# Optimization experiments

Hardware: AMD Instinct MI355X
Metric: run time of the kernel (lower is better)

The kernel has to match this reference:

```python
import math
import jax
import jax.numpy as jnp
import numpy as np
from jax import lax

B, L, D = 8, 3072, 512
DM, H, CF = 512, 8, 512
E = DM // H
KSIZE = 25
C_FACTOR = 1


def setup_inputs() -> dict:
    key = jax.random.key(0)
    ks = jax.random.split(key, 16)
    s = lambda fan: 1.0 / np.sqrt(fan)
    inp = {
        "inputs": jax.random.normal(ks[0], (B, L, D), jnp.float32),
        "W_res": jax.random.normal(ks[1], (D, DM), jnp.float32) * s(D),
        "b_res": jnp.zeros((DM,), jnp.float32),
        "W_in": jax.random.normal(ks[2], (DM, DM), jnp.float32) * s(DM),
        "b_in": jnp.zeros((DM,), jnp.float32),
        "Wq": jax.random.normal(ks[3], (DM, DM), jnp.float32) * s(DM),
        "bq": jnp.zeros((DM,), jnp.float32),
        "Wk": jax.random.normal(ks[4], (DM, DM), jnp.float32) * s(DM),
        "bk": jnp.zeros((DM,), jnp.float32),
        "Wv": jax.random.normal(ks[5], (DM, DM), jnp.float32) * s(DM),
        "bv": jnp.zeros((DM,), jnp.float32),
        "Wo": jax.random.normal(ks[6], (DM, DM), jnp.float32) * s(DM),
        "bo": jnp.zeros((DM,), jnp.float32),
        "Wc1": jax.random.normal(ks[7], (DM, CF), jnp.float32) * s(DM),
        "Wc2": jax.random.normal(ks[8], (CF, CF), jnp.float32) * s(CF),
    }
    return inp


def series_decomp(x):
    # moving average with 'same' padding, TF-style (count excludes padding)
    ssum = lax.reduce_window(x, 0.0, lax.add, (1, KSIZE, 1), (1, 1, 1), "SAME")
    cnt = lax.reduce_window(jnp.ones_like(x), 0.0, lax.add, (1, KSIZE, 1), (1, 1, 1), "SAME")
    trend = ssum / cnt
    return x - trend, trend


def auto_correlation(q, k, v):
    # q,k,v: [B, L, H, E]
    qf = jnp.fft.rfft(q, axis=1)
    kf = jnp.fft.rfft(k, axis=1)
    corr = jnp.fft.irfft(qf * jnp.conj(kf), n=L, axis=1)  # [B, L, H, E]
    mean_corr = corr.mean(axis=(2, 3))  # [B, L]
    k_top = int(C_FACTOR * math.log(L))  # = 8
    weights, delays = lax.top_k(mean_corr, k_top)  # [B, k_top]
    w = jax.nn.softmax(weights, axis=-1)  # [B, k_top]
    # gather v rolled by each delay: idx[b,i,l] = (l + delay[b,i]) % L
    idx = (jnp.arange(L)[None, None, :] + delays[:, :, None]) % L  # [B, k_top, L]
    v_rolled = jnp.take_along_axis(v[:, None], idx[:, :, :, None, None], axis=2)  # [B,k,L,H,E]
    return jnp.einsum("bklhe,bk->blhe", v_rolled, w)


def reference(inputs, W_res, b_res, W_in, b_in, Wq, bq, Wk, bk, Wv, bv, Wo, bo, Wc1, Wc2):
    proj = inputs @ W_res + b_res  # [B,L,DM]
    x = proj @ W_in + b_in
    q = (x @ Wq + bq).reshape(B, L, H, E)
    kk = (x @ Wk + bk).reshape(B, L, H, E)
    vv = (x @ Wv + bv).reshape(B, L, H, E)
    attn = auto_correlation(q, kk, vv).reshape(B, L, DM)
    attn = attn @ Wo + bo
    x = attn + proj
    seasonal, _ = series_decomp(x)
    y = jax.nn.relu(seasonal @ Wc1)  # Conv1D kernel_size=1, no bias
    y = y @ Wc2
    out, _ = series_decomp(y)
    return out
```

## Files before the change

### kernel.cpp

```cpp
#include <hip/hip_runtime.h>
#include <hip/hip_bf16.h>


#define LQ 3072
#define DD 512
#define BB 8
#define MTOT (BB * LQ)
#define KTOP 8
#define KSZ 25
#define KHALF 12
#define KK 512
#define KB (KK * 2)

typedef unsigned short ushort_t;
typedef __attribute__((ext_vector_type(4))) float f32x4;
typedef __attribute__((ext_vector_type(8))) short s16x8;
typedef __attribute__((ext_vector_type(4))) short s16x4;

typedef __attribute__((address_space(1))) unsigned int u32_g;
typedef __attribute__((address_space(3))) unsigned int u32_l;

__device__ __forceinline__ ushort_t f2bfbits(float x) {
  __hip_bfloat16 h = __float2bfloat16(x);
  return __builtin_bit_cast(unsigned short, h);
}
__device__ __forceinline__ float bfbits2f(ushort_t s) {
  __hip_bfloat16 h = __builtin_bit_cast(__hip_bfloat16, (unsigned short)s);
  return __bfloat162float(h);
}

__device__ __forceinline__ void gload_lds16(const void* g, void* l) {
  __builtin_amdgcn_global_load_lds((const u32_g*)g, (u32_l*)l, 16, 0, 0);
}

__device__ __forceinline__ void gemm3_core(
    const ushort_t* __restrict__ Ah, const ushort_t* __restrict__ Al,
    const ushort_t* __restrict__ Bh, const ushort_t* __restrict__ Bl,
    int arow0, int brow0, char* lds, f32x4 acc[4][4]) {
  const int tid = threadIdx.x, lane = tid & 63, w = tid >> 6;
  const int wr = w >> 1, wc = w & 1;
  const int c = lane & 15, qd = lane >> 4;

  const ushort_t* ssrc = (w == 0) ? Ah : (w == 1) ? Al : (w == 2) ? Bh : Bl;
  const int srow0 = (w < 2) ? arow0 : brow0;
  const int L0 = lane >> 3, sl = lane & 7;
  const int u = sl ^ L0;
  const char* gbase =
      (const char*)ssrc + (size_t)(srow0 + 2 * L0 + (u >> 2)) * KB + (u & 3) * 16;
  char* ldsT = lds + w * 8192;

  int aoff[4], boff[4];
#pragma unroll
  for (int m = 0; m < 4; m++) {
    int r = wr * 64 + m * 16 + c;
    int L = r >> 1;
    aoff[m] = L * 128 + (((((r & 1) << 2) | qd) ^ (L & 7)) << 4);
    r = wc * 64 + m * 16 + c;
    L = r >> 1;
    boff[m] = 16384 + L * 128 + (((((r & 1) << 2) | qd) ^ (L & 7)) << 4);
  }

#pragma unroll
  for (int m = 0; m < 4; m++)
#pragma unroll
    for (int n = 0; n < 4; n++) acc[m][n] = 0.f;

  for (int k0 = 0; k0 < KK; k0 += 32) {
    __syncthreads();
    const char* g = gbase + k0 * 2;
#pragma unroll
    for (int i = 0; i < 8; i++) gload_lds16(g + (size_t)i * (16 * KB), ldsT + i * 1024);
    __syncthreads();

    s16x8 ah[4], al[4];
#pragma unroll
    for (int m = 0; m < 4; m++) {
      ah[m] = *(const s16x8*)(lds + aoff[m]);
      al[m] = *(const s16x8*)(lds + 8192 + aoff[m]);
    }
#pragma unroll
    for (int n = 0; n < 4; n++) {
      s16x8 bh = *(const s16x8*)(lds + boff[n]);
      s16x8 bl = *(const s16x8*)(lds + 8192 + boff[n]);
#pragma unroll
      for (int m = 0; m < 4; m++) {
        acc[m][n] = __builtin_amdgcn_mfma_f32_16x16x32_bf16(ah[m], bh, acc[m][n], 0, 0, 0);
        acc[m][n] = __builtin_amdgcn_mfma_f32_16x16x32_bf16(ah[m], bl, acc[m][n], 0, 0, 0);
        acc[m][n] = __builtin_amdgcn_mfma_f32_16x16x32_bf16(al[m], bh, acc[m][n], 0, 0, 0);
      }
    }
  }
}

template <int OUTMODE, int RESMODE, int RELU>
__global__ __launch_bounds__(256, 3) void gemm_bf16x3(
    const ushort_t* __restrict__ Ah, const ushort_t* __restrict__ Al,
    const ushort_t* __restrict__ Bh, const ushort_t* __restrict__ Bl,
    const float* __restrict__ bias,
    const ushort_t* __restrict__ resH, const ushort_t* __restrict__ resL,
    float* __restrict__ outF, ushort_t* __restrict__ outH, ushort_t* __restrict__ outL) {
  __shared__ alignas(16) char lds[32768];
  const int m0 = blockIdx.y * 128, n0 = blockIdx.x * 128;
  f32x4 acc[4][4];
  gemm3_core(Ah, Al, Bh, Bl, m0, n0, lds, acc);

  const int tid = threadIdx.x, lane = tid & 63, w = tid >> 6;
  const int wr = w >> 1, wc = w & 1, qd = lane >> 4, c = lane & 15;
#pragma unroll
  for (int m = 0; m < 4; m++)
#pragma unroll
    for (int n = 0; n < 4; n++) {
      int col = n0 + wc * 64 + n * 16 + c;
      float badd = bias ? bias[col] : 0.f;
#pragma unroll
      for (int r = 0; r < 4; r++) {
        int row = m0 + wr * 64 + m * 16 + 4 * qd + r;
        size_t off = (size_t)row * DD + col;
        float val = acc[m][n][r] + badd;
        if (RESMODE == 1) val += bfbits2f(resH[off]) + bfbits2f(resL[off]);
        if (RELU) val = fmaxf(val, 0.f);
        if (OUTMODE == 0) {
          outF[off] = val;
        } else {
          ushort_t h = f2bfbits(val);
          outH[off] = h;
          outL[off] = f2bfbits(val - bfbits2f(h));
        }
      }
    }
}

__global__ __launch_bounds__(256, 3) void corr_gemm(
    const ushort_t* __restrict__ Qh, const ushort_t* __restrict__ Ql,
    const ushort_t* __restrict__ Kh, const ushort_t* __restrict__ Kl,
    float* __restrict__ mc) {
  __shared__ alignas(16) char lds[32768];
  __shared__ float bins[256];
  const int b = blockIdx.z;
  const int m0 = blockIdx.y * 128, n0 = blockIdx.x * 128;
  bins[threadIdx.x] = 0.f;
  f32x4 acc[4][4];
  gemm3_core(Qh, Ql, Kh, Kl, b * LQ + m0, b * LQ + n0, lds, acc);

  const int tid = threadIdx.x, lane = tid & 63, w = tid >> 6;
  const int wr = w >> 1, wc = w & 1, qd = lane >> 4, c = lane & 15;

  float psum[7][4];
#pragma unroll
  for (int d = 0; d < 7; d++)
#pragma unroll
    for (int r = 0; r < 4; r++) psum[d][r] = 0.f;
#pragma unroll
  for (int m = 0; m < 4; m++)
#pragma unroll
    for (int n = 0; n < 4; n++) {
      int d = m - n + 3;
#pragma unroll
      for (int r = 0; r < 4; r++) psum[d][r] += acc[m][n][r];
    }

  __syncthreads();
  const int lanebase = 64 * (wr - wc) + 4 * qd - c + 127;
#pragma unroll
  for (int d = 0; d < 7; d++)
#pragma unroll
    for (int r = 0; r < 4; r++) atomicAdd(&bins[lanebase + 16 * (d - 3) + r], psum[d][r]);
  __syncthreads();

  if (tid < 255) {
    int tau = 128 * ((int)blockIdx.y - (int)blockIdx.x) + tid - 127;
    tau = ((tau % LQ) + LQ) % LQ;
    atomicAdd(&mc[b * LQ + tau], bins[tid]);
  }
}

struct P8 {
  const float* p[8];
};

__global__ void transpose_split(P8 srcs, ushort_t* __restrict__ dH, ushort_t* __restrict__ dL) {
  __shared__ float t[32][33];
  const int i = blockIdx.z;
  const float* src = srcs.p[i];
  const size_t base = (size_t)i * DD * DD;
  const int x0 = blockIdx.x * 32, y0 = blockIdx.y * 32;
  const int tx = threadIdx.x, ty = threadIdx.y;
#pragma unroll
  for (int j = 0; j < 4; j++) t[ty + 8 * j][tx] = src[(size_t)(y0 + ty + 8 * j) * DD + x0 + tx];
  __syncthreads();
#pragma unroll
  for (int j = 0; j < 4; j++) {
    float v = t[tx][ty + 8 * j];
    size_t o = base + (size_t)(x0 + ty + 8 * j) * DD + (y0 + tx);
    ushort_t h = f2bfbits(v);
    dH[o] = h;
    dL[o] = f2bfbits(v - bfbits2f(h));
  }
}

__global__ void split_f32(const float* __restrict__ x, ushort_t* __restrict__ h,
                          ushort_t* __restrict__ l, int n4) {
  int i = blockIdx.x * blockDim.x + threadIdx.x;
  if (i >= n4) return;
  f32x4 v = *reinterpret_cast<const f32x4*>(x + (size_t)i * 4);
  s16x4 hv, lv;
#pragma unroll
  for (int j = 0; j < 4; j++) {
    ushort_t hb = f2bfbits(v[j]);
    hv[j] = (short)hb;
    lv[j] = (short)f2bfbits(v[j] - bfbits2f(hb));
  }
  *reinterpret_cast<s16x4*>(h + (size_t)i * 4) = hv;
  *reinterpret_cast<s16x4*>(l + (size_t)i * 4) = lv;
}

__global__ void zero_f32(float* __restrict__ p, int n) {
  int i = blockIdx.x * blockDim.x + threadIdx.x;
  if (i < n) p[i] = 0.f;
}

__global__ void topk_softmax(const float* __restrict__ mc, int* __restrict__ delays,
                             float* __restrict__ weights) {
  const int b = blockIdx.x, tid = threadIdx.x;
  __shared__ float vals[LQ];
  __shared__ float rv[256];
  __shared__ int ri[256];
  __shared__ float topv[KTOP];
  __shared__ int topi[KTOP];
  for (int i = tid; i < LQ; i += 256) vals[i] = mc[b * LQ + i] * (1.0f / 512.0f);
  __syncthreads();
  for (int t = 0; t < KTOP; t++) {
    float bv = -1e30f;
    int bi = 0x7fffffff;
    for (int i = tid; i < LQ; i += 256) {
      float v = vals[i];
      if (v > bv || (v == bv && i < bi)) { bv = v; bi = i; }
    }
    rv[tid] = bv;
    ri[tid] = bi;
    __syncthreads();
    for (int s = 128; s > 0; s >>= 1) {
      if (tid < s) {
        if (rv[tid + s] > rv[tid] || (rv[tid + s] == rv[tid] && ri[tid + s] < ri[tid])) {
          rv[tid] = rv[tid + s];
          ri[tid] = ri[tid + s];
        }
      }
      __syncthreads();
    }
    if (tid == 0) {
      topv[t] = rv[0];
      topi[t] = ri[0];
      vals[ri[0]] = -1e38f;
    }
    __syncthreads();
  }
  if (tid == 0) {
    float mx = topv[0];
#pragma unroll
    for (int i = 1; i < KTOP; i++) mx = fmaxf(mx, topv[i]);
    float e[KTOP], s = 0.f;
#pragma unroll
    for (int i = 0; i < KTOP; i++) {
      e[i] = expf(topv[i] - mx);
      s += e[i];
    }
#pragma unroll
    for (int i = 0; i < KTOP; i++) {
      weights[b * KTOP + i] = e[i] / s;
      delays[b * KTOP + i] = topi[i];
    }
  }
}

__global__ void attn_gather(const float* __restrict__ v, const int* __restrict__ delays,
                            const float* __restrict__ w, ushort_t* __restrict__ oH,
                            ushort_t* __restrict__ oL) {
  int idx = blockIdx.x * blockDim.x + threadIdx.x;
  const int total = BB * LQ * (DD / 4);
  if (idx >= total) return;
  int b = idx / (LQ * (DD / 4));
  int rem = idx % (LQ * (DD / 4));
  int l = rem / (DD / 4), dq = rem % (DD / 4);
  f32x4 acc = 0.f;
#pragma unroll
  for (int i = 0; i < KTOP; i++) {
    int d = delays[b * KTOP + i];
    float wi = w[b * KTOP + i];
    int ls = (l + d) % LQ;
    f32x4 vv = *reinterpret_cast<const f32x4*>(v + ((size_t)b * LQ + ls) * DD + dq * 4);
    acc += vv * wi;
  }
  size_t o = ((size_t)b * LQ + l) * DD + dq * 4;
  s16x4 hv, lv;
#pragma unroll
  for (int j = 0; j < 4; j++) {
    ushort_t hb = f2bfbits(acc[j]);
    hv[j] = (short)hb;
    lv[j] = (short)f2bfbits(acc[j] - bfbits2f(hb));
  }
  *reinterpret_cast<s16x4*>(oH + o) = hv;
  *reinterpret_cast<s16x4*>(oL + o) = lv;
}

template <int OUT_HL>
__global__ void decomp_kernel(const float* __restrict__ x, float* __restrict__ outF,
                              ushort_t* __restrict__ outH, ushort_t* __restrict__ outL) {
  __shared__ float tile[64 + 2 * KHALF][64];
  const int l0 = blockIdx.x * 64, d0 = blockIdx.y * 64, b = blockIdx.z;
  const int tx = threadIdx.x & 63, ty = threadIdx.x >> 6;
  const float* xb = x + (size_t)b * LQ * DD;
  for (int r = ty; r < 64 + 2 * KHALF; r += 4) {
    int l = l0 + r - KHALF;
    tile[r][tx] = (l >= 0 && l < LQ) ? xb[(size_t)l * DD + d0 + tx] : 0.f;
  }
  __syncthreads();
#pragma unroll
  for (int j = 0; j < 16; j++) {
    int lr = ty + 4 * j;
    int l = l0 + lr;
    float s = 0.f;
#pragma unroll
    for (int t = 0; t < KSZ; t++) s += tile[lr + t][tx];
    int lo = max(0, l - KHALF), hi = min(LQ - 1, l + KHALF);
    float val = tile[lr + KHALF][tx] - s / (float)(hi - lo + 1);
    size_t o = ((size_t)b * LQ + l) * DD + d0 + tx;
    if (OUT_HL) {
      ushort_t h = f2bfbits(val);
      outH[o] = h;
      outL[o] = f2bfbits(val - bfbits2f(h));
    } else {
      outF[o] = val;
    }
  }
}

extern "C" void kernel_launch(void* const* d_in, const int* in_sizes, int n_in,
                              void* d_out, int out_size, void* d_ws, size_t ws_size,
                              hipStream_t stream) {
  const float* inputs = (const float*)d_in[0];
  const float* b_res = (const float*)d_in[2];
  const float* b_in = (const float*)d_in[4];
  const float* bq = (const float*)d_in[6];
  const float* bk = (const float*)d_in[8];
  const float* bv = (const float*)d_in[10];
  const float* bo = (const float*)d_in[12];
  float* outp = (float*)d_out;

  char* ws = (char*)d_ws;
  ushort_t* WTh = (ushort_t*)ws;
  ushort_t* WTl = (ushort_t*)(ws + (4u << 20));
  float* mean_corr = (float*)(ws + (8u << 20));
  int* delays = (int*)(ws + (8u << 20) + 98304);
  float* weights = (float*)(ws + (8u << 20) + 98304 + 256);
  char* R0 = ws + (16u << 20);
  char* R1 = ws + (64u << 20);
  char* R2 = ws + (112u << 20);
  char* R3 = ws + (160u << 20);
  const size_t HALF = 24u << 20;
  ushort_t *R0h = (ushort_t*)R0, *R0l = (ushort_t*)(R0 + HALF);
  ushort_t *R1h = (ushort_t*)R1, *R1l = (ushort_t*)(R1 + HALF);
  ushort_t *R2h = (ushort_t*)R2, *R2l = (ushort_t*)(R2 + HALF);
  ushort_t *R3h = (ushort_t*)R3, *R3l = (ushort_t*)(R3 + HALF);
  const size_t WS1 = (size_t)DD * DD;

  P8 wp;
  wp.p[0] = (const float*)d_in[1];
  wp.p[1] = (const float*)d_in[3];
  wp.p[2] = (const float*)d_in[5];
  wp.p[3] = (const float*)d_in[7];
  wp.p[4] = (const float*)d_in[9];
  wp.p[5] = (const float*)d_in[11];
  wp.p[6] = (const float*)d_in[13];
  wp.p[7] = (const float*)d_in[14];

  transpose_split<<<dim3(16, 16, 8), dim3(32, 8), 0, stream>>>(wp, WTh, WTl);
  split_f32<<<(MTOT * DD / 4 + 255) / 256, 256, 0, stream>>>(inputs, R1h, R1l, MTOT * DD / 4);

  const dim3 G(DD / 128, MTOT / 128);
  gemm_bf16x3<1, 0, 0><<<G, 256, 0, stream>>>(R1h, R1l, WTh + 0 * WS1, WTl + 0 * WS1, b_res,
                                              nullptr, nullptr, nullptr, R0h, R0l);
  gemm_bf16x3<1, 0, 0><<<G, 256, 0, stream>>>(R0h, R0l, WTh + 1 * WS1, WTl + 1 * WS1, b_in,
                                              nullptr, nullptr, nullptr, R1h, R1l);
  gemm_bf16x3<1, 0, 0><<<G, 256, 0, stream>>>(R1h, R1l, WTh + 2 * WS1, WTl + 2 * WS1, bq,
                                              nullptr, nullptr, nullptr, R2h, R2l);
  gemm_bf16x3<1, 0, 0><<<G, 256, 0, stream>>>(R1h, R1l, WTh + 3 * WS1, WTl + 3 * WS1, bk,
                                              nullptr, nullptr, nullptr, R3h, R3l);
  zero_f32<<<(BB * LQ + 255) / 256, 256, 0, stream>>>(mean_corr, BB * LQ);
  corr_gemm<<<dim3(LQ / 128, LQ / 128, BB), 256, 0, stream>>>(R2h, R2l, R3h, R3l, mean_corr);
  topk_softmax<<<BB, 256, 0, stream>>>(mean_corr, delays, weights);
  gemm_bf16x3<0, 0, 0><<<G, 256, 0, stream>>>(R1h, R1l, WTh + 4 * WS1, WTl + 4 * WS1, bv,
                                              nullptr, nullptr, (float*)R2, nullptr, nullptr);
  attn_gather<<<(BB * LQ * (DD / 4) + 255) / 256, 256, 0, stream>>>((const float*)R2, delays,
                                                                    weights, R3h, R3l);
  gemm_bf16x3<0, 1, 0><<<G, 256, 0, stream>>>(R3h, R3l, WTh + 5 * WS1, WTl + 5 * WS1, bo,
                                              R0h, R0l, (float*)R1, nullptr, nullptr);
  decomp_kernel<1><<<dim3(LQ / 64, DD / 64, BB), 256, 0, stream>>>((const float*)R1, nullptr,
                                                                   R0h, R0l);
  gemm_bf16x3<1, 0, 1><<<G, 256, 0, stream>>>(R0h, R0l, WTh + 6 * WS1, WTl + 6 * WS1, nullptr,
                                              nullptr, nullptr, nullptr, R2h, R2l);
  gemm_bf16x3<0, 0, 0><<<G, 256, 0, stream>>>(R2h, R2l, WTh + 7 * WS1, WTl + 7 * WS1, nullptr,
                                              nullptr, nullptr, (float*)R1, nullptr, nullptr);
  decomp_kernel<0><<<dim3(LQ / 64, DD / 64, BB), 256, 0, stream>>>((const float*)R1, outp,
                                                                   nullptr, nullptr);
}
```

Before: 1.015 ms.

## Pipeline bf16x3 GEMM core with triple-buffered LDS and 256x128 tiles

```diff
diff --git a/kernel.cpp b/kernel.cpp
--- a/kernel.cpp
+++ b/kernel.cpp
@@ -11,6 +11,8 @@
 #define KHALF 12
 #define KK 512
 #define KB (KK * 2)
+#define SLOT 49152
+#define NT 16
 
 typedef unsigned short ushort_t;
 typedef __attribute__((ext_vector_type(4))) float f32x4;
@@ -33,31 +35,43 @@
   __builtin_amdgcn_global_load_lds((const u32_g*)g, (u32_l*)l, 16, 0, 0);
 }
 
-__device__ __forceinline__ void gemm3_core(
-    const ushort_t* __restrict__ Ah, const ushort_t* __restrict__ Al,
-    const ushort_t* __restrict__ Bh, const ushort_t* __restrict__ Bl,
+#define MFMA3(m, n)                                                                       \
+  acc[m][n] = __builtin_amdgcn_mfma_f32_16x16x32_bf16(ah[m], bh[n], acc[m][n], 0, 0, 0); \
+  acc[m][n] = __builtin_amdgcn_mfma_f32_16x16x32_bf16(ah[m], bl[n], acc[m][n], 0, 0, 0); \
+  acc[m][n] = __builtin_amdgcn_mfma_f32_16x16x32_bf16(al[m], bh[n], acc[m][n], 0, 0, 0);
+
+__device__ __forceinline__ void core256(
+    const ushort_t* __restrict__ Ahp, const ushort_t* __restrict__ Alp,
+    const ushort_t* __restrict__ Bhp, const ushort_t* __restrict__ Blp,
     int arow0, int brow0, char* lds, f32x4 acc[4][4]) {
   const int tid = threadIdx.x, lane = tid & 63, w = tid >> 6;
-  const int wr = w >> 1, wc = w & 1;
+  const int wm = w >> 1, wn = w & 1;
   const int c = lane & 15, qd = lane >> 4;
-
-  const ushort_t* ssrc = (w == 0) ? Ah : (w == 1) ? Al : (w == 2) ? Bh : Bl;
-  const int srow0 = (w < 2) ? arow0 : brow0;
-  const int L0 = lane >> 3, sl = lane & 7;
-  const int u = sl ^ L0;
-  const char* gbase =
-      (const char*)ssrc + (size_t)(srow0 + 2 * L0 + (u >> 2)) * KB + (u & 3) * 16;
-  char* ldsT = lds + w * 8192;
-
-  int aoff[4], boff[4];
+  const int L0 = lane >> 3, sl = lane & 7, u = sl ^ L0;
+
+  const char* gp[6];
+  int lo[6];
+#pragma unroll
+  for (int i = 0; i < 6; i++) {
+    int g = 6 * w + i;
+    const ushort_t* src;
+    int tbase, cin, rbase;
+    if (g < 16)      { src = Ahp; tbase = 0;     cin = g;      rbase = arow0; }
+    else if (g < 32) { src = Alp; tbase = 16384; cin = g - 16; rbase = arow0; }
+    else if (g < 40) { src = Bhp; tbase = 32768; cin = g - 32; rbase = brow0; }
+    else             { src = Blp; tbase = 40960; cin = g - 40; rbase = brow0; }
+    gp[i] = (const char*)src + (size_t)(rbase + 16 * cin + 2 * L0 + (u >> 2)) * KB +
+            (u & 3) * 16;
+    lo[i] = tbase + cin * 1024;
+  }
+
+  int aoh[4], boh[4];
 #pragma unroll
   for (int m = 0; m < 4; m++) {
-    int r = wr * 64 + m * 16 + c;
-    int L = r >> 1;
-    aoff[m] = L * 128 + (((((r & 1) << 2) | qd) ^ (L & 7)) << 4);
-    r = wc * 64 + m * 16 + c;
-    L = r >> 1;
-    boff[m] = 16384 + L * 128 + (((((r & 1) << 2) | qd) ^ (L & 7)) << 4);
+    int r = wm * 64 + m * 16 + c, L = r >> 1;
+    aoh[m] = L * 128 + (((((r & 1) << 2) | qd) ^ (L & 7)) << 4);
+    int rb = wn * 64 + m * 16 + c, Lb = rb >> 1;
+    boh[m] = 32768 + Lb * 128 + (((((rb & 1) << 2) | qd) ^ (Lb & 7)) << 4);
   }
 
 #pragma unroll
@@ -65,56 +79,91 @@
 #pragma unroll
     for (int n = 0; n < 4; n++) acc[m][n] = 0.f;
 
-  for (int k0 = 0; k0 < KK; k0 += 32) {
-    __syncthreads();
-    const char* g = gbase + k0 * 2;
-#pragma unroll
-    for (int i = 0; i < 8; i++) gload_lds16(g + (size_t)i * (16 * KB), ldsT + i * 1024);
-    __syncthreads();
-
-    s16x8 ah[4], al[4];
+#pragma unroll
+  for (int i = 0; i < 6; i++) gload_lds16(gp[i], lds + lo[i]);
+#pragma unroll
+  for (int i = 0; i < 6; i++) gload_lds16(gp[i] + 64, lds + SLOT + lo[i]);
+
+  int sb = 0, sb2 = 2 * SLOT;
+  for (int t = 0; t < NT; t++) {
+    if (t < NT - 1) asm volatile("s_waitcnt vmcnt(6)" ::: "memory");
+    else            asm volatile("s_waitcnt vmcnt(0)" ::: "memory");
+    __builtin_amdgcn_s_barrier();
+    __builtin_amdgcn_sched_barrier(0);
+
+    const char* lb = lds + sb;
+    s16x8 ah[4], al[4], bh[4], bl[4];
+    if (t + 2 < NT) {
+      const int go = (t + 2) * 64;
+#pragma unroll
+      for (int i = 0; i < 3; i++) gload_lds16(gp[i] + go, lds + sb2 + lo[i]);
+    }
 #pragma unroll
     for (int m = 0; m < 4; m++) {
-      ah[m] = *(const s16x8*)(lds + aoff[m]);
-      al[m] = *(const s16x8*)(lds + 8192 + aoff[m]);
-    }
-#pragma unroll
-    for (int n = 0; n < 4; n++) {
-      s16x8 bh = *(const s16x8*)(lds + boff[n]);
-      s16x8 bl = *(const s16x8*)(lds + 8192 + boff[n]);
-#pragma unroll
-      for (int m = 0; m < 4; m++) {
-        acc[m][n] = __builtin_amdgcn_mfma_f32_16x16x32_bf16(ah[m], bh, acc[m][n], 0, 0, 0);
-        acc[m][n] = __builtin_amdgcn_mfma_f32_16x16x32_bf16(ah[m], bl, acc[m][n], 0, 0, 0);
-        acc[m][n] = __builtin_amdgcn_mfma_f32_16x16x32_bf16(al[m], bh, acc[m][n], 0, 0, 0);
-      }
-    }
+      ah[m] = *(const s16x8*)(lb + aoh[m]);
+      al[m] = *(const s16x8*)(lb + aoh[m] + 16384);
+    }
+#pragma unroll
+    for (int n = 0; n < 2; n++) {
+      bh[n] = *(const s16x8*)(lb + boh[n]);
+      bl[n] = *(const s16x8*)(lb + boh[n] + 8192);
+    }
+    __builtin_amdgcn_s_barrier();
+    __builtin_amdgcn_s_setprio(1);
+#pragma unroll
+    for (int n = 0; n < 2; n++) {
+#pragma unroll
+      for (int m = 0; m < 4; m++) { MFMA3(m, n) }
+    }
+    __builtin_amdgcn_s_setprio(0);
+    __builtin_amdgcn_s_barrier();
+    if (t + 2 < NT) {
+      const int go = (t + 2) * 64;
+#pragma unroll
+      for (int i = 3; i < 6; i++) gload_lds16(gp[i] + go, lds + sb2 + lo[i]);
+    }
+#pragma unroll
+    for (int n = 2; n < 4; n++) {
+      bh[n] = *(const s16x8*)(lb + boh[n]);
+      bl[n] = *(const s16x8*)(lb + boh[n] + 8192);
+    }
+    __builtin_amdgcn_s_barrier();
+    __builtin_amdgcn_s_setprio(1);
+#pragma unroll
+    for (int n = 2; n < 4; n++) {
+#pragma unroll
+      for (int m = 0; m < 4; m++) { MFMA3(m, n) }
+    }
+    __builtin_amdgcn_s_setprio(0);
+
+    sb += SLOT;  if (sb == 3 * SLOT)  sb = 0;
+    sb2 += SLOT; if (sb2 == 3 * SLOT) sb2 = 0;
   }
 }
 
 template <int OUTMODE, int RESMODE, int RELU>
-__global__ __launch_bounds__(256, 3) void gemm_bf16x3(
+__global__ __launch_bounds__(512, 2) void gemm_bf16x3(
     const ushort_t* __restrict__ Ah, const ushort_t* __restrict__ Al,
     const ushort_t* __restrict__ Bh, const ushort_t* __restrict__ Bl,
     const float* __restrict__ bias,
     const ushort_t* __restrict__ resH, const ushort_t* __restrict__ resL,
     float* __restrict__ outF, ushort_t* __restrict__ outH, ushort_t* __restrict__ outL) {
-  __shared__ alignas(16) char lds[32768];
-  const int m0 = blockIdx.y * 128, n0 = blockIdx.x * 128;
+  __shared__ alignas(16) char lds[3 * SLOT];
+  const int m0 = blockIdx.y * 256, n0 = blockIdx.x * 128;
   f32x4 acc[4][4];
-  gemm3_core(Ah, Al, Bh, Bl, m0, n0, lds, acc);
+  core256(Ah, Al, Bh, Bl, m0, n0, lds, acc);
 
   const int tid = threadIdx.x, lane = tid & 63, w = tid >> 6;
-  const int wr = w >> 1, wc = w & 1, qd = lane >> 4, c = lane & 15;
+  const int wm = w >> 1, wn = w & 1, qd = lane >> 4, c = lane & 15;
 #pragma unroll
   for (int m = 0; m < 4; m++)
 #pragma unroll
     for (int n = 0; n < 4; n++) {
-      int col = n0 + wc * 64 + n * 16 + c;
+      int col = n0 + wn * 64 + n * 16 + c;
       float badd = bias ? bias[col] : 0.f;
 #pragma unroll
       for (int r = 0; r < 4; r++) {
-        int row = m0 + wr * 64 + m * 16 + 4 * qd + r;
+        int row = m0 + wm * 64 + m * 16 + 4 * qd + r;
         size_t off = (size_t)row * DD + col;
         float val = acc[m][n][r] + badd;
         if (RESMODE == 1) val += bfbits2f(resH[off]) + bfbits2f(resL[off]);
@@ -130,20 +179,20 @@
     }
 }
 
-__global__ __launch_bounds__(256, 3) void corr_gemm(
+__global__ __launch_bounds__(512, 2) void corr_gemm(
     const ushort_t* __restrict__ Qh, const ushort_t* __restrict__ Ql,
     const ushort_t* __restrict__ Kh, const ushort_t* __restrict__ Kl,
     float* __restrict__ mc) {
-  __shared__ alignas(16) char lds[32768];
-  __shared__ float bins[256];
+  __shared__ alignas(16) char lds[3 * SLOT];
+  __shared__ float bins[383];
   const int b = blockIdx.z;
-  const int m0 = blockIdx.y * 128, n0 = blockIdx.x * 128;
-  bins[threadIdx.x] = 0.f;
+  const int m0 = blockIdx.y * 256, n0 = blockIdx.x * 128;
+  if (threadIdx.x < 383) bins[threadIdx.x] = 0.f;
   f32x4 acc[4][4];
-  gemm3_core(Qh, Ql, Kh, Kl, b * LQ + m0, b * LQ + n0, lds, acc);
+  core256(Qh, Ql, Kh, Kl, b * LQ + m0, b * LQ + n0, lds, acc);
 
   const int tid = threadIdx.x, lane = tid & 63, w = tid >> 6;
-  const int wr = w >> 1, wc = w & 1, qd = lane >> 4, c = lane & 15;
+  const int wm = w >> 1, wn = w & 1, qd = lane >> 4, c = lane & 15;
 
   float psum[7][4];
 #pragma unroll
@@ -159,16 +208,15 @@
       for (int r = 0; r < 4; r++) psum[d][r] += acc[m][n][r];
     }
 
-  __syncthreads();
-  const int lanebase = 64 * (wr - wc) + 4 * qd - c + 127;
+  const int lanebase = 64 * wm - 64 * wn + 4 * qd - c + 127;
 #pragma unroll
   for (int d = 0; d < 7; d++)
 #pragma unroll
     for (int r = 0; r < 4; r++) atomicAdd(&bins[lanebase + 16 * (d - 3) + r], psum[d][r]);
   __syncthreads();
 
-  if (tid < 255) {
-    int tau = 128 * ((int)blockIdx.y - (int)blockIdx.x) + tid - 127;
+  if (tid < 383) {
+    int tau = 256 * (int)blockIdx.y - 128 * (int)blockIdx.x + tid - 127;
     tau = ((tau % LQ) + LQ) % LQ;
     atomicAdd(&mc[b * LQ + tau], bins[tid]);
   }
@@ -377,29 +425,29 @@
   transpose_split<<<dim3(16, 16, 8), dim3(32, 8), 0, stream>>>(wp, WTh, WTl);
   split_f32<<<(MTOT * DD / 4 + 255) / 256, 256, 0, stream>>>(inputs, R1h, R1l, MTOT * DD / 4);
 
-  const dim3 G(DD / 128, MTOT / 128);
-  gemm_bf16x3<1, 0, 0><<<G, 256, 0, stream>>>(R1h, R1l, WTh + 0 * WS1, WTl + 0 * WS1, b_res,
+  const dim3 G(DD / 128, MTOT / 256);
+  gemm_bf16x3<1, 0, 0><<<G, 512, 0, stream>>>(R1h, R1l, WTh + 0 * WS1, WTl + 0 * WS1, b_res,
                                               nullptr, nullptr, nullptr, R0h, R0l);
-  gemm_bf16x3<1, 0, 0><<<G, 256, 0, stream>>>(R0h, R0l, WTh + 1 * WS1, WTl + 1 * WS1, b_in,
+  gemm_bf16x3<1, 0, 0><<<G, 512, 0, stream>>>(R0h, R0l, WTh + 1 * WS1, WTl + 1 * WS1, b_in,
                                               nullptr, nullptr, nullptr, R1h, R1l);
-  gemm_bf16x3<1, 0, 0><<<G, 256, 0, stream>>>(R1h, R1l, WTh + 2 * WS1, WTl + 2 * WS1, bq,
+  gemm_bf16x3<1, 0, 0><<<G, 512, 0, stream>>>(R1h, R1l, WTh + 2 * WS1, WTl + 2 * WS1, bq,
                                               nullptr, nullptr, nullptr, R2h, R2l);
-  gemm_bf16x3<1, 0, 0><<<G, 256, 0, stream>>>(R1h, R1l, WTh + 3 * WS1, WTl + 3 * WS1, bk,
+  gemm_bf16x3<1, 0, 0><<<G, 512, 0, stream>>>(R1h, R1l, WTh + 3 * WS1, WTl + 3 * WS1, bk,
                                               nullptr, nullptr, nullptr, R3h, R3l);
   zero_f32<<<(BB * LQ + 255) / 256, 256, 0, stream>>>(mean_corr, BB * LQ);
-  corr_gemm<<<dim3(LQ / 128, LQ / 128, BB), 256, 0, stream>>>(R2h, R2l, R3h, R3l, mean_corr);
+  corr_gemm<<<dim3(LQ / 128, LQ / 256, BB), 512, 0, stream>>>(R2h, R2l, R3h, R3l, mean_corr);
   topk_softmax<<<BB, 256, 0, stream>>>(mean_corr, delays, weights);
-  gemm_bf16x3<0, 0, 0><<<G, 256, 0, stream>>>(R1h, R1l, WTh + 4 * WS1, WTl + 4 * WS1, bv,
+  gemm_bf16x3<0, 0, 0><<<G, 512, 0, stream>>>(R1h, R1l, WTh + 4 * WS1, WTl + 4 * WS1, bv,
                                               nullptr, nullptr, (float*)R2, nullptr, nullptr);
   attn_gather<<<(BB * LQ * (DD / 4) + 255) / 256, 256, 0, stream>>>((const float*)R2, delays,
                                                                     weights, R3h, R3l);
-  gemm_bf16x3<0, 1, 0><<<G, 256, 0, stream>>>(R3h, R3l, WTh + 5 * WS1, WTl + 5 * WS1, bo,
+  gemm_bf16x3<0, 1, 0><<<G, 512, 0, stream>>>(R3h, R3l, WTh + 5 * WS1, WTl + 5 * WS1, bo,
                                               R0h, R0l, (float*)R1, nullptr, nullptr);
   decomp_kernel<1><<<dim3(LQ / 64, DD / 64, BB), 256, 0, stream>>>((const float*)R1, nullptr,
                                                                    R0h, R0l);
-  gemm_bf16x3<1, 0, 1><<<G, 256, 0, stream>>>(R0h, R0l, WTh + 6 * WS1, WTl + 6 * WS1, nullptr,
+  gemm_bf16x3<1, 0, 1><<<G, 512, 0, stream>>>(R0h, R0l, WTh + 6 * WS1, WTl + 6 * WS1, nullptr,
                                               nullptr, nullptr, nullptr, R2h, R2l);
-  gemm_bf16x3<0, 0, 0><<<G, 256, 0, stream>>>(R2h, R2l, WTh + 7 * WS1, WTl + 7 * WS1, nullptr,
+  gemm_bf16x3<0, 0, 0><<<G, 512, 0, stream>>>(R2h, R2l, WTh + 7 * WS1, WTl + 7 * WS1, nullptr,
                                               nullptr, nullptr, (float*)R1, nullptr, nullptr);
   decomp_kernel<0><<<dim3(LQ / 64, DD / 64, BB), 256, 0, stream>>>((const float*)R1, outp,
                                                                    nullptr, nullptr);
```

Measured after the change: 1.124 ms. 1.11x slower.
